# Performance work log

Hardware: AMD Instinct MI355X
Metric: run time of the kernel (lower is better)

Reference implementation:

```python
import jax, jax.numpy as jnp
import numpy as np

N_NODES = 50000
N_EDGES = 800000
DIM_IN, DIM_H, DIM_OUT = 128, 128, 64


def _init_linear(key, fan_in, fan_out):
    # kaiming-uniform-ish init, matches torch Linear scale
    lim = 1.0 / np.sqrt(fan_in)
    return jax.random.uniform(key, (fan_in, fan_out), jnp.float32, -lim, lim)


def setup_inputs() -> dict:
    key = jax.random.key(0)
    ks = jax.random.split(key, 12)
    x = jax.random.normal(ks[0], (N_NODES, DIM_IN), jnp.float32)
    edge_index = jax.random.randint(ks[1], (2, N_EDGES), 0, N_NODES, jnp.int32)
    dims = [(DIM_IN, DIM_H), (DIM_H, DIM_H), (DIM_H, DIM_OUT)]
    inp = {"x": x, "edge_index": edge_index}
    for i, (fi, fo) in enumerate(dims):
        inp[f"Wl{i}"] = _init_linear(ks[2 + 3 * i], fi, fo)   # neighbor transform
        inp[f"Wr{i}"] = _init_linear(ks[3 + 3 * i], fi, fo)   # root transform
        inp[f"b{i}"] = jnp.zeros((fo,), jnp.float32)
    return inp


def _sage_layer(x, src, dst, Wl, Wr, b):
    # mean aggregation of neighbor messages x[src] at destination nodes
    msg = x[src]                                              # [E, d]
    agg = jax.ops.segment_sum(msg, dst, num_segments=N_NODES)  # [N, d]
    cnt = jax.ops.segment_sum(jnp.ones((src.shape[0],), x.dtype), dst,
                              num_segments=N_NODES)
    mean = agg / jnp.maximum(cnt, 1.0)[:, None]               # isolated nodes -> 0
    return mean @ Wl + b + x @ Wr                              # SAGEConv


def reference(x, edge_index, Wl0, Wr0, b0, Wl1, Wr1, b1, Wl2, Wr2, b2):
    src, dst = edge_index[0], edge_index[1]
    layers = [(Wl0, Wr0, b0), (Wl1, Wr1, b1), (Wl2, Wr2, b2)]
    h = x
    for i, (Wl, Wr, b) in enumerate(layers):
        h = _sage_layer(h, src, dst, Wl, Wr, b)
        if i != len(layers) - 1:
            h = jax.nn.relu(h)  # dropout p=0.2 is identity in eval mode
    return jax.nn.log_softmax(h, axis=1), h
```

## Files before the change

kernel.cpp:

```cpp
#include <hip/hip_runtime.h>

#define N_NODES 50000
#define N_EDGES 800000
#define SCAN_BLOCKS 196
#define WIN 6250

typedef __attribute__((ext_vector_type(8))) short short8;
typedef __attribute__((ext_vector_type(4))) float f32x4;
typedef unsigned short ushort_t;
typedef unsigned int uint_t;

__device__ inline ushort_t f2bf(float f) {
    union { float f; uint_t u; } v; v.f = f;
    uint_t u = v.u;
    u += 0x7fffu + ((u >> 16) & 1u);
    return (ushort_t)(u >> 16);
}
__device__ inline float bflo(uint_t v) { return __uint_as_float(v << 16); }
__device__ inline float bfhi(uint_t v) { return __uint_as_float(v & 0xffff0000u); }
__device__ inline float bf2f(ushort_t v) { return __uint_as_float((uint_t)v << 16); }

__global__ void count_edges_mp(const int* __restrict__ ei, int* __restrict__ cnt) {
    int g = blockIdx.x & 7;
    int nb = gridDim.x >> 3;
    int bi = blockIdx.x >> 3;
    int lo = g * WIN;
    for (int e = bi * 256 + threadIdx.x; e < N_EDGES; e += nb * 256) {
        int d = ei[N_EDGES + e];
        if ((unsigned)(d - lo) < WIN) atomicAdd(&cnt[d], 1);
    }
}

__global__ void fill_csr_mp(const int* __restrict__ ei, int* __restrict__ cursor,
                            int* __restrict__ csr_src) {
    int g = blockIdx.x & 7;
    int nb = gridDim.x >> 3;
    int bi = blockIdx.x >> 3;
    int lo = g * WIN;
    for (int e = bi * 256 + threadIdx.x; e < N_EDGES; e += nb * 256) {
        int d = ei[N_EDGES + e];
        if ((unsigned)(d - lo) < WIN) {
            int p = atomicAdd(&cursor[d], 1);
            csr_src[p] = ei[e];
        }
    }
}

__global__ void block_sums(const int* __restrict__ cnt, int* __restrict__ bsum) {
    int i = blockIdx.x * 256 + threadIdx.x;
    int v = (i < N_NODES) ? cnt[i] : 0;
    for (int off = 32; off; off >>= 1) v += __shfl_down(v, off, 64);
    __shared__ int s[4];
    if ((threadIdx.x & 63) == 0) s[threadIdx.x >> 6] = v;
    __syncthreads();
    if (threadIdx.x == 0) bsum[blockIdx.x] = s[0] + s[1] + s[2] + s[3];
}

__global__ void scan_bsums(const int* __restrict__ bsum, int* __restrict__ bprefix,
                           int* __restrict__ rowstart) {
    __shared__ int s[256];
    int t = threadIdx.x;
    int v = (t < SCAN_BLOCKS) ? bsum[t] : 0;
    s[t] = v;
    __syncthreads();
    for (int off = 1; off < 256; off <<= 1) {
        int add = (t >= off) ? s[t - off] : 0;
        __syncthreads();
        s[t] += add;
        __syncthreads();
    }
    bprefix[t] = s[t] - v;
    if (t == 0) rowstart[N_NODES] = N_EDGES;
}

__global__ void apply_scan(const int* __restrict__ cnt, const int* __restrict__ bprefix,
                           int* __restrict__ rowstart, int* __restrict__ cursor) {
    __shared__ int s[256];
    int t = threadIdx.x;
    int i = blockIdx.x * 256 + t;
    int v = (i < N_NODES) ? cnt[i] : 0;
    s[t] = v;
    __syncthreads();
    for (int off = 1; off < 256; off <<= 1) {
        int add = (t >= off) ? s[t - off] : 0;
        __syncthreads();
        s[t] += add;
        __syncthreads();
    }
    int excl = s[t] - v + bprefix[blockIdx.x];
    if (i < N_NODES) { rowstart[i] = excl; cursor[i] = excl; }
}

__global__ void cvt_bf16(const float* __restrict__ in, ushort_t* __restrict__ out, int n4) {
    int i = blockIdx.x * 256 + threadIdx.x;
    if (i < n4) {
        float4 v = ((const float4*)in)[i];
        ushort4 o;
        o.x = f2bf(v.x); o.y = f2bf(v.y); o.z = f2bf(v.z); o.w = f2bf(v.w);
        ((ushort4*)out)[i] = o;
    }
}

__global__ void pack_w256(const float* __restrict__ Wl, const float* __restrict__ Wr,
                          ushort_t* __restrict__ out) {
    int idx = blockIdx.x * 256 + threadIdx.x;
    if (idx >= 8 * 8 * 64 * 8) return;
    int j = idx & 7, l = (idx >> 3) & 63, t = (idx >> 9) & 7, ks = idx >> 12;
    int n = t * 16 + (l & 15);
    int k = ks * 32 + (l >> 4) * 8 + j;
    float w = (k < 128) ? Wl[k * 128 + n] : Wr[(k - 128) * 128 + n];
    out[idx] = f2bf(w);
}

__global__ void pack_wzr(const float* __restrict__ Wl, const float* __restrict__ Wr,
                         ushort_t* __restrict__ out) {
    int idx = blockIdx.x * 256 + threadIdx.x;
    if (idx >= 4 * 8 * 64 * 8) return;
    int j = idx & 7, l = (idx >> 3) & 63, t = (idx >> 9) & 7, ks = idx >> 12;
    int n = t * 16 + (l & 15);
    int k = ks * 32 + (l >> 4) * 8 + j;
    float w = (n < 64) ? Wl[k * 64 + n] : Wr[k * 64 + (n - 64)];
    out[idx] = f2bf(w);
}

__global__ void aggregate_bf(const ushort_t* __restrict__ hbf,
                             const int* __restrict__ rowstart,
                             const int* __restrict__ csr_src,
                             ushort_t* __restrict__ meanbf) {
    int node = blockIdx.x * 4 + (threadIdx.x >> 6);
    int lane = threadIdx.x & 63;
    if (node >= N_NODES) return;
    int s0 = rowstart[node], s1 = rowstart[node + 1];
    float ax = 0.f, ay = 0.f;
    const uint_t* base = (const uint_t*)hbf;
    for (int b = s0; b < s1; b += 64) {
        int m = min(64, s1 - b);
        int idx = (lane < m) ? csr_src[b + lane] : 0;
        int j = 0;
        for (; j + 8 <= m; j += 8) {
            uint_t v0 = base[(size_t)__shfl(idx, j + 0, 64) * 64 + lane];
            uint_t v1 = base[(size_t)__shfl(idx, j + 1, 64) * 64 + lane];
            uint_t v2 = base[(size_t)__shfl(idx, j + 2, 64) * 64 + lane];
            uint_t v3 = base[(size_t)__shfl(idx, j + 3, 64) * 64 + lane];
            uint_t v4 = base[(size_t)__shfl(idx, j + 4, 64) * 64 + lane];
            uint_t v5 = base[(size_t)__shfl(idx, j + 5, 64) * 64 + lane];
            uint_t v6 = base[(size_t)__shfl(idx, j + 6, 64) * 64 + lane];
            uint_t v7 = base[(size_t)__shfl(idx, j + 7, 64) * 64 + lane];
            ax += ((bflo(v0) + bflo(v1)) + (bflo(v2) + bflo(v3)))
                + ((bflo(v4) + bflo(v5)) + (bflo(v6) + bflo(v7)));
            ay += ((bfhi(v0) + bfhi(v1)) + (bfhi(v2) + bfhi(v3)))
                + ((bfhi(v4) + bfhi(v5)) + (bfhi(v6) + bfhi(v7)));
        }
        for (; j < m; ++j) {
            uint_t v = base[(size_t)__shfl(idx, j, 64) * 64 + lane];
            ax += bflo(v);
            ay += bfhi(v);
        }
    }
    float inv = 1.0f / fmaxf((float)(s1 - s0), 1.0f);
    ax *= inv; ay *= inv;
    uint_t packed = (uint_t)f2bf(ax) | ((uint_t)f2bf(ay) << 16);
    ((uint_t*)meanbf)[(size_t)node * 64 + lane] = packed;
}

__global__ __launch_bounds__(256) void sage_gemm_pk(
    const ushort_t* __restrict__ mean_bf, const ushort_t* __restrict__ root_bf,
    const ushort_t* __restrict__ Bpk, const float* __restrict__ bias,
    ushort_t* __restrict__ out_bf) {
    int lane = threadIdx.x & 63;
    int wave = threadIdx.x >> 6;
    int row16 = lane & 15;
    int quad = lane >> 4;
    int rowBase = blockIdx.x * 64 + wave * 16;
    int arow = min(rowBase + row16, N_NODES - 1);
    const ushort_t* mrow = mean_bf + (size_t)arow * 128;
    const ushort_t* rrow = root_bf + (size_t)arow * 128;
    const short8* bp = (const short8*)Bpk + lane;

    f32x4 acc[8];
    #pragma unroll
    for (int t = 0; t < 8; ++t) { f32x4 z = {0.f, 0.f, 0.f, 0.f}; acc[t] = z; }

    #pragma unroll
    for (int ks = 0; ks < 8; ++ks) {
        const ushort_t* src = (ks < 4) ? (mrow + ks * 32 + quad * 8)
                                       : (rrow + (ks - 4) * 32 + quad * 8);
        short8 afrag = *(const short8*)src;
        #pragma unroll
        for (int t = 0; t < 8; ++t) {
            short8 bfrag = bp[(ks * 8 + t) * 64];
            acc[t] = __builtin_amdgcn_mfma_f32_16x16x32_bf16(afrag, bfrag, acc[t], 0, 0, 0);
        }
    }

    #pragma unroll
    for (int t = 0; t < 8; ++t) {
        int col = t * 16 + row16;
        float bv = bias[col];
        #pragma unroll
        for (int r = 0; r < 4; ++r) {
            int row = rowBase + quad * 4 + r;
            if (row < N_NODES) {
                float v = fmaxf(acc[t][r] + bv, 0.f);
                out_bf[(size_t)row * 128 + col] = f2bf(v);
            }
        }
    }
}

__global__ __launch_bounds__(256) void gemm_zr_pk(
    const ushort_t* __restrict__ h_bf, const ushort_t* __restrict__ Bpk,
    const float* __restrict__ bias,
    ushort_t* __restrict__ z_bf, float* __restrict__ r_f32) {
    int lane = threadIdx.x & 63;
    int wave = threadIdx.x >> 6;
    int row16 = lane & 15;
    int quad = lane >> 4;
    int rowBase = blockIdx.x * 64 + wave * 16;
    int arow = min(rowBase + row16, N_NODES - 1);
    const ushort_t* hrow = h_bf + (size_t)arow * 128;
    const short8* bp = (const short8*)Bpk + lane;

    f32x4 acc[8];
    #pragma unroll
    for (int t = 0; t < 8; ++t) { f32x4 z = {0.f, 0.f, 0.f, 0.f}; acc[t] = z; }

    #pragma unroll
    for (int ks = 0; ks < 4; ++ks) {
        short8 afrag = *(const short8*)(hrow + ks * 32 + quad * 8);
        #pragma unroll
        for (int t = 0; t < 8; ++t) {
            short8 bfrag = bp[(ks * 8 + t) * 64];
            acc[t] = __builtin_amdgcn_mfma_f32_16x16x32_bf16(afrag, bfrag, acc[t], 0, 0, 0);
        }
    }

    #pragma unroll
    for (int t = 0; t < 8; ++t) {
        int col = t * 16 + row16;
        #pragma unroll
        for (int r = 0; r < 4; ++r) {
            int row = rowBase + quad * 4 + r;
            if (row < N_NODES) {
                if (col < 64) {
                    z_bf[(size_t)row * 64 + col] = f2bf(acc[t][r]);
                } else {
                    r_f32[(size_t)row * 64 + (col - 64)] = acc[t][r] + bias[col - 64];
                }
            }
        }
    }
}

__global__ void final_agg_softmax(const ushort_t* __restrict__ z_bf,
                                  const float* __restrict__ r_f32,
                                  const int* __restrict__ rowstart,
                                  const int* __restrict__ csr_src,
                                  float* __restrict__ out) {
    int node = blockIdx.x * 4 + (threadIdx.x >> 6);
    int lane = threadIdx.x & 63;
    if (node >= N_NODES) return;
    int s0 = rowstart[node], s1 = rowstart[node + 1];
    float a = 0.f;
    for (int b = s0; b < s1; b += 64) {
        int m = min(64, s1 - b);
        int idx = (lane < m) ? csr_src[b + lane] : 0;
        int j = 0;
        for (; j + 8 <= m; j += 8) {
            float v0 = bf2f(z_bf[(size_t)__shfl(idx, j + 0, 64) * 64 + lane]);
            float v1 = bf2f(z_bf[(size_t)__shfl(idx, j + 1, 64) * 64 + lane]);
            float v2 = bf2f(z_bf[(size_t)__shfl(idx, j + 2, 64) * 64 + lane]);
            float v3 = bf2f(z_bf[(size_t)__shfl(idx, j + 3, 64) * 64 + lane]);
            float v4 = bf2f(z_bf[(size_t)__shfl(idx, j + 4, 64) * 64 + lane]);
            float v5 = bf2f(z_bf[(size_t)__shfl(idx, j + 5, 64) * 64 + lane]);
            float v6 = bf2f(z_bf[(size_t)__shfl(idx, j + 6, 64) * 64 + lane]);
            float v7 = bf2f(z_bf[(size_t)__shfl(idx, j + 7, 64) * 64 + lane]);
            a += ((v0 + v1) + (v2 + v3)) + ((v4 + v5) + (v6 + v7));
        }
        for (; j < m; ++j)
            a += bf2f(z_bf[(size_t)__shfl(idx, j, 64) * 64 + lane]);
    }
    float inv = 1.0f / fmaxf((float)(s1 - s0), 1.0f);
    float h = a * inv + r_f32[(size_t)node * 64 + lane];
    float mx = h;
    for (int off = 32; off; off >>= 1) mx = fmaxf(mx, __shfl_xor(mx, off, 64));
    float e = expf(h - mx);
    float s = e;
    for (int off = 32; off; off >>= 1) s += __shfl_xor(s, off, 64);
    float lse = mx + logf(s);
    out[(size_t)node * 64 + lane] = h - lse;
    out[(size_t)N_NODES * 64 + (size_t)node * 64 + lane] = h;
}

extern "C" void kernel_launch(void* const* d_in, const int* in_sizes, int n_in,
                              void* d_out, int out_size, void* d_ws, size_t ws_size,
                              hipStream_t stream) {
    const float* x  = (const float*)d_in[0];
    const int* ei   = (const int*)d_in[1];
    const float* Wl0 = (const float*)d_in[2];
    const float* Wr0 = (const float*)d_in[3];
    const float* b0  = (const float*)d_in[4];
    const float* Wl1 = (const float*)d_in[5];
    const float* Wr1 = (const float*)d_in[6];
    const float* b1  = (const float*)d_in[7];
    const float* Wl2 = (const float*)d_in[8];
    const float* Wr2 = (const float*)d_in[9];
    const float* b2  = (const float*)d_in[10];
    float* out = (float*)d_out;

    char* ws = (char*)d_ws;
    int* cnt      = (int*)(ws + 0x000000);
    int* rowstart = (int*)(ws + 0x040000);
    int* cursor   = (int*)(ws + 0x080000);
    int* bsum     = (int*)(ws + 0x0C0000);
    int* bprefix  = (int*)(ws + 0x0C1000);
    int* csr_src  = (int*)(ws + 0x100000);
    ushort_t* pk0 = (ushort_t*)(ws + 0x420000);
    ushort_t* pk1 = (ushort_t*)(ws + 0x440000);
    ushort_t* pkz = (ushort_t*)(ws + 0x460000);
    ushort_t* x_bf    = (ushort_t*)(ws + 0x0500000);
    ushort_t* mean_bf = (ushort_t*)(ws + 0x1200000);
    ushort_t* h_bf    = (ushort_t*)(ws + 0x1F00000);
    ushort_t* z_bf    = (ushort_t*)(ws + 0x1200000);
    float*    r_f32   = (float*)  (ws + 0x0500000);

    pack_w256<<<128, 256, 0, stream>>>(Wl0, Wr0, pk0);
    pack_w256<<<128, 256, 0, stream>>>(Wl1, Wr1, pk1);
    pack_wzr<<<64, 256, 0, stream>>>(Wl2, Wr2, pkz);

    hipMemsetAsync(cnt, 0, N_NODES * sizeof(int), stream);
    count_edges_mp<<<1024, 256, 0, stream>>>(ei, cnt);
    block_sums<<<SCAN_BLOCKS, 256, 0, stream>>>(cnt, bsum);
    scan_bsums<<<1, 256, 0, stream>>>(bsum, bprefix, rowstart);
    apply_scan<<<SCAN_BLOCKS, 256, 0, stream>>>(cnt, bprefix, rowstart, cursor);
    fill_csr_mp<<<1024, 256, 0, stream>>>(ei, cursor, csr_src);

    cvt_bf16<<<6250, 256, 0, stream>>>(x, x_bf, (N_NODES * 128) / 4);

    aggregate_bf<<<12500, 256, 0, stream>>>(x_bf, rowstart, csr_src, mean_bf);
    sage_gemm_pk<<<782, 256, 0, stream>>>(mean_bf, x_bf, pk0, b0, h_bf);

    aggregate_bf<<<12500, 256, 0, stream>>>(h_bf, rowstart, csr_src, mean_bf);
    sage_gemm_pk<<<782, 256, 0, stream>>>(mean_bf, h_bf, pk1, b1, h_bf);

    gemm_zr_pk<<<782, 256, 0, stream>>>(h_bf, pkz, b2, z_bf, r_f32);
    final_agg_softmax<<<12500, 256, 0, stream>>>(z_bf, r_f32, rowstart, csr_src, out);
}
```

Before: 329.8 us.

## Fuse mean aggregation into SAGE GEMM via LDS and vectorize gathers

Neighbor aggregation is now done inside the GEMM kernel. Each wave gathers 16 nodes' neighbor rows with 16-byte loads across four 16-lane groups and writes the bf16 means to LDS, which feed the MFMA A-fragments directly. This removes the mean_bf round trip through global memory and one launch per layer, and the buffers are reassigned so layer 1 no longer writes its output in place over its input. The final aggregation plus softmax packs 8 nodes per wave with uint4 gathers and float4 stores. The cost is only 782 blocks for the gather phase, which lowers latency hiding, and lane-divergent degree loops.

```diff
diff --git a/kernel.cpp b/kernel.cpp
--- a/kernel.cpp
+++ b/kernel.cpp
@@ -19,6 +19,11 @@
 __device__ inline float bflo(uint_t v) { return __uint_as_float(v << 16); }
 __device__ inline float bfhi(uint_t v) { return __uint_as_float(v & 0xffff0000u); }
 __device__ inline float bf2f(ushort_t v) { return __uint_as_float((uint_t)v << 16); }
+
+#define ACC8(V) { a[0] += bflo((V).x); a[1] += bfhi((V).x); \
+                  a[2] += bflo((V).y); a[3] += bfhi((V).y); \
+                  a[4] += bflo((V).z); a[5] += bfhi((V).z); \
+                  a[6] += bflo((V).w); a[7] += bfhi((V).w); }
 
 __global__ void count_edges_mp(const int* __restrict__ ei, int* __restrict__ cnt) {
     int g = blockIdx.x & 7;
@@ -123,58 +128,69 @@
     out[idx] = f2bf(w);
 }
 
-__global__ void aggregate_bf(const ushort_t* __restrict__ hbf,
-                             const int* __restrict__ rowstart,
-                             const int* __restrict__ csr_src,
-                             ushort_t* __restrict__ meanbf) {
-    int node = blockIdx.x * 4 + (threadIdx.x >> 6);
-    int lane = threadIdx.x & 63;
-    if (node >= N_NODES) return;
-    int s0 = rowstart[node], s1 = rowstart[node + 1];
-    float ax = 0.f, ay = 0.f;
-    const uint_t* base = (const uint_t*)hbf;
-    for (int b = s0; b < s1; b += 64) {
-        int m = min(64, s1 - b);
-        int idx = (lane < m) ? csr_src[b + lane] : 0;
-        int j = 0;
-        for (; j + 8 <= m; j += 8) {
-            uint_t v0 = base[(size_t)__shfl(idx, j + 0, 64) * 64 + lane];
-            uint_t v1 = base[(size_t)__shfl(idx, j + 1, 64) * 64 + lane];
-            uint_t v2 = base[(size_t)__shfl(idx, j + 2, 64) * 64 + lane];
-            uint_t v3 = base[(size_t)__shfl(idx, j + 3, 64) * 64 + lane];
-            uint_t v4 = base[(size_t)__shfl(idx, j + 4, 64) * 64 + lane];
-            uint_t v5 = base[(size_t)__shfl(idx, j + 5, 64) * 64 + lane];
-            uint_t v6 = base[(size_t)__shfl(idx, j + 6, 64) * 64 + lane];
-            uint_t v7 = base[(size_t)__shfl(idx, j + 7, 64) * 64 + lane];
-            ax += ((bflo(v0) + bflo(v1)) + (bflo(v2) + bflo(v3)))
-                + ((bflo(v4) + bflo(v5)) + (bflo(v6) + bflo(v7)));
-            ay += ((bfhi(v0) + bfhi(v1)) + (bfhi(v2) + bfhi(v3)))
-                + ((bfhi(v4) + bfhi(v5)) + (bfhi(v6) + bfhi(v7)));
-        }
-        for (; j < m; ++j) {
-            uint_t v = base[(size_t)__shfl(idx, j, 64) * 64 + lane];
-            ax += bflo(v);
-            ay += bfhi(v);
-        }
-    }
-    float inv = 1.0f / fmaxf((float)(s1 - s0), 1.0f);
-    ax *= inv; ay *= inv;
-    uint_t packed = (uint_t)f2bf(ax) | ((uint_t)f2bf(ay) << 16);
-    ((uint_t*)meanbf)[(size_t)node * 64 + lane] = packed;
-}
-
-__global__ __launch_bounds__(256) void sage_gemm_pk(
-    const ushort_t* __restrict__ mean_bf, const ushort_t* __restrict__ root_bf,
+__global__ __launch_bounds__(256) void sage_fused(
+    const ushort_t* __restrict__ feat_bf,
+    const int* __restrict__ rowstart,
+    const int* __restrict__ csr_src,
     const ushort_t* __restrict__ Bpk, const float* __restrict__ bias,
     ushort_t* __restrict__ out_bf) {
+    __shared__ uint_t mlds[64][68];
     int lane = threadIdx.x & 63;
     int wave = threadIdx.x >> 6;
+    int rowBase = blockIdx.x * 64 + wave * 16;
+    int sub = lane >> 4;
+    int sl  = lane & 15;
+    int gb  = sub << 4;
+    const uint_t* base = (const uint_t*)feat_bf;
+
+    for (int p = 0; p < 4; ++p) {
+        int node = rowBase + p * 4 + sub;
+        int s0 = 0, s1 = 0;
+        if (node < N_NODES) { s0 = rowstart[node]; s1 = rowstart[node + 1]; }
+        float a[8];
+        #pragma unroll
+        for (int k = 0; k < 8; ++k) a[k] = 0.f;
+
+        int pos = s0;
+        while (__any(pos < s1)) {
+            int m = min(16, s1 - pos);
+            int idxr = (sl < m) ? csr_src[pos + sl] : 0;
+            int mm = max(m, 0);
+            mm = max(mm, __shfl_xor(mm, 16, 64));
+            mm = max(mm, __shfl_xor(mm, 32, 64));
+            for (int j = 0; j < mm; j += 8) {
+                int  sidx[8];
+                bool vld[8];
+                #pragma unroll
+                for (int k = 0; k < 8; ++k) {
+                    int q = __shfl(idxr, (gb + j + k) & 63, 64);
+                    vld[k]  = (j + k < m);
+                    sidx[k] = vld[k] ? q : 0;
+                }
+                uint4 V[8];
+                #pragma unroll
+                for (int k = 0; k < 8; ++k)
+                    V[k] = *(const uint4*)(base + (size_t)sidx[k] * 64 + (sl << 2));
+                #pragma unroll
+                for (int k = 0; k < 8; ++k)
+                    if (vld[k]) { ACC8(V[k]); }
+            }
+            pos += 16;
+        }
+        float inv = 1.0f / fmaxf((float)(s1 - s0), 1.0f);
+        uint4 o;
+        o.x = (uint_t)f2bf(a[0] * inv) | ((uint_t)f2bf(a[1] * inv) << 16);
+        o.y = (uint_t)f2bf(a[2] * inv) | ((uint_t)f2bf(a[3] * inv) << 16);
+        o.z = (uint_t)f2bf(a[4] * inv) | ((uint_t)f2bf(a[5] * inv) << 16);
+        o.w = (uint_t)f2bf(a[6] * inv) | ((uint_t)f2bf(a[7] * inv) << 16);
+        *((uint4*)&mlds[wave * 16 + p * 4 + sub][sl << 2]) = o;
+    }
+    __syncthreads();
+
     int row16 = lane & 15;
-    int quad = lane >> 4;
-    int rowBase = blockIdx.x * 64 + wave * 16;
-    int arow = min(rowBase + row16, N_NODES - 1);
-    const ushort_t* mrow = mean_bf + (size_t)arow * 128;
-    const ushort_t* rrow = root_bf + (size_t)arow * 128;
+    int quad  = lane >> 4;
+    int arow  = min(rowBase + row16, N_NODES - 1);
+    const ushort_t* rrow = feat_bf + (size_t)arow * 128;
     const short8* bp = (const short8*)Bpk + lane;
 
     f32x4 acc[8];
@@ -183,9 +199,11 @@
 
     #pragma unroll
     for (int ks = 0; ks < 8; ++ks) {
-        const ushort_t* src = (ks < 4) ? (mrow + ks * 32 + quad * 8)
-                                       : (rrow + (ks - 4) * 32 + quad * 8);
-        short8 afrag = *(const short8*)src;
+        short8 afrag;
+        if (ks < 4)
+            afrag = *(const short8*)&mlds[wave * 16 + row16][ks * 16 + quad * 4];
+        else
+            afrag = *(const short8*)(rrow + (ks - 4) * 32 + quad * 8);
         #pragma unroll
         for (int t = 0; t < 8; ++t) {
             short8 bfrag = bp[(ks * 8 + t) * 64];
@@ -252,44 +270,75 @@
     }
 }
 
-__global__ void final_agg_softmax(const ushort_t* __restrict__ z_bf,
-                                  const float* __restrict__ r_f32,
-                                  const int* __restrict__ rowstart,
-                                  const int* __restrict__ csr_src,
-                                  float* __restrict__ out) {
-    int node = blockIdx.x * 4 + (threadIdx.x >> 6);
+__global__ __launch_bounds__(256) void final_agg_softmax2(
+    const ushort_t* __restrict__ z_bf, const float* __restrict__ r_f32,
+    const int* __restrict__ rowstart, const int* __restrict__ csr_src,
+    float* __restrict__ out) {
     int lane = threadIdx.x & 63;
+    int wave = threadIdx.x >> 6;
+    int sub = lane >> 3;
+    int sl  = lane & 7;
+    int gb  = sub << 3;
+    int node = blockIdx.x * 32 + wave * 8 + sub;
+    int s0 = 0, s1 = 0;
+    if (node < N_NODES) { s0 = rowstart[node]; s1 = rowstart[node + 1]; }
+
+    float a[8];
+    #pragma unroll
+    for (int k = 0; k < 8; ++k) a[k] = 0.f;
+    const uint_t* zb = (const uint_t*)z_bf;
+
+    int pos = s0;
+    while (__any(pos < s1)) {
+        int m = min(8, s1 - pos);
+        int idxr = (sl < m) ? csr_src[pos + sl] : 0;
+        int  sidx[8];
+        bool vld[8];
+        #pragma unroll
+        for (int k = 0; k < 8; ++k) {
+            int q = __shfl(idxr, (gb + k) & 63, 64);
+            vld[k]  = (k < m);
+            sidx[k] = vld[k] ? q : 0;
+        }
+        uint4 V[8];
+        #pragma unroll
+        for (int k = 0; k < 8; ++k)
+            V[k] = *(const uint4*)(zb + (size_t)sidx[k] * 32 + (sl << 2));
+        #pragma unroll
+        for (int k = 0; k < 8; ++k)
+            if (vld[k]) { ACC8(V[k]); }
+        pos += 8;
+    }
     if (node >= N_NODES) return;
-    int s0 = rowstart[node], s1 = rowstart[node + 1];
-    float a = 0.f;
-    for (int b = s0; b < s1; b += 64) {
-        int m = min(64, s1 - b);
-        int idx = (lane < m) ? csr_src[b + lane] : 0;
-        int j = 0;
-        for (; j + 8 <= m; j += 8) {
-            float v0 = bf2f(z_bf[(size_t)__shfl(idx, j + 0, 64) * 64 + lane]);
-            float v1 = bf2f(z_bf[(size_t)__shfl(idx, j + 1, 64) * 64 + lane]);
-            float v2 = bf2f(z_bf[(size_t)__shfl(idx, j + 2, 64) * 64 + lane]);
-            float v3 = bf2f(z_bf[(size_t)__shfl(idx, j + 3, 64) * 64 + lane]);
-            float v4 = bf2f(z_bf[(size_t)__shfl(idx, j + 4, 64) * 64 + lane]);
-            float v5 = bf2f(z_bf[(size_t)__shfl(idx, j + 5, 64) * 64 + lane]);
-            float v6 = bf2f(z_bf[(size_t)__shfl(idx, j + 6, 64) * 64 + lane]);
-            float v7 = bf2f(z_bf[(size_t)__shfl(idx, j + 7, 64) * 64 + lane]);
-            a += ((v0 + v1) + (v2 + v3)) + ((v4 + v5) + (v6 + v7));
-        }
-        for (; j < m; ++j)
-            a += bf2f(z_bf[(size_t)__shfl(idx, j, 64) * 64 + lane]);
-    }
+
     float inv = 1.0f / fmaxf((float)(s1 - s0), 1.0f);
-    float h = a * inv + r_f32[(size_t)node * 64 + lane];
-    float mx = h;
-    for (int off = 32; off; off >>= 1) mx = fmaxf(mx, __shfl_xor(mx, off, 64));
-    float e = expf(h - mx);
-    float s = e;
-    for (int off = 32; off; off >>= 1) s += __shfl_xor(s, off, 64);
+    const float4* rr = (const float4*)(r_f32 + (size_t)node * 64 + sl * 8);
+    float4 rA = rr[0], rB = rr[1];
+    float h[8];
+    h[0] = a[0] * inv + rA.x; h[1] = a[1] * inv + rA.y;
+    h[2] = a[2] * inv + rA.z; h[3] = a[3] * inv + rA.w;
+    h[4] = a[4] * inv + rB.x; h[5] = a[5] * inv + rB.y;
+    h[6] = a[6] * inv + rB.z; h[7] = a[7] * inv + rB.w;
+
+    float mx = fmaxf(fmaxf(fmaxf(h[0], h[1]), fmaxf(h[2], h[3])),
+                     fmaxf(fmaxf(h[4], h[5]), fmaxf(h[6], h[7])));
+    mx = fmaxf(mx, __shfl_xor(mx, 1, 64));
+    mx = fmaxf(mx, __shfl_xor(mx, 2, 64));
+    mx = fmaxf(mx, __shfl_xor(mx, 4, 64));
+    float s = 0.f;
+    #pragma unroll
+    for (int k = 0; k < 8; ++k) s += expf(h[k] - mx);
+    s += __shfl_xor(s, 1, 64);
+    s += __shfl_xor(s, 2, 64);
+    s += __shfl_xor(s, 4, 64);
     float lse = mx + logf(s);
-    out[(size_t)node * 64 + lane] = h - lse;
-    out[(size_t)N_NODES * 64 + (size_t)node * 64 + lane] = h;
+
+    size_t o1 = (size_t)node * 64 + sl * 8;
+    size_t o2 = (size_t)N_NODES * 64 + o1;
+    *(float4*)(out + o1)     = make_float4(h[0] - lse, h[1] - lse, h[2] - lse, h[3] - lse);
+    *(float4*)(out + o1 + 4) = make_float4(h[4] - lse, h[5] - lse, h[6] - lse, h[7] - lse);
+    *(float4*)(out + o2)     = make_float4(h[0], h[1], h[2], h[3]);
+    *(float4*)(out + o2 + 4) = make_float4(h[4], h[5], h[6], h[7]);
 }
 
 extern "C" void kernel_launch(void* const* d_in, const int* in_sizes, int n_in,
@@ -318,11 +367,11 @@
     ushort_t* pk0 = (ushort_t*)(ws + 0x420000);
     ushort_t* pk1 = (ushort_t*)(ws + 0x440000);
     ushort_t* pkz = (ushort_t*)(ws + 0x460000);
-    ushort_t* x_bf    = (ushort_t*)(ws + 0x0500000);
-    ushort_t* mean_bf = (ushort_t*)(ws + 0x1200000);
-    ushort_t* h_bf    = (ushort_t*)(ws + 0x1F00000);
-    ushort_t* z_bf    = (ushort_t*)(ws + 0x1200000);
-    float*    r_f32   = (float*)  (ws + 0x0500000);
+    ushort_t* x_bf  = (ushort_t*)(ws + 0x0500000);
+    ushort_t* h_bf  = (ushort_t*)(ws + 0x1200000);
+    ushort_t* h2_bf = (ushort_t*)(ws + 0x1F00000);
+    ushort_t* z_bf  = (ushort_t*)(ws + 0x0500000);
+    float*    r_f32 = (float*)  (ws + 0x1200000);
 
     pack_w256<<<128, 256, 0, stream>>>(Wl0, Wr0, pk0);
     pack_w256<<<128, 256, 0, stream>>>(Wl1, Wr1, pk1);
@@ -337,12 +386,10 @@
 
     cvt_bf16<<<6250, 256, 0, stream>>>(x, x_bf, (N_NODES * 128) / 4);
 
-    aggregate_bf<<<12500, 256, 0, stream>>>(x_bf, rowstart, csr_src, mean_bf);
-    sage_gemm_pk<<<782, 256, 0, stream>>>(mean_bf, x_bf, pk0, b0, h_bf);
-
-    aggregate_bf<<<12500, 256, 0, stream>>>(h_bf, rowstart, csr_src, mean_bf);
-    sage_gemm_pk<<<782, 256, 0, stream>>>(mean_bf, h_bf, pk1, b1, h_bf);
-
-    gemm_zr_pk<<<782, 256, 0, stream>>>(h_bf, pkz, b2, z_bf, r_f32);
-    final_agg_softmax<<<12500, 256, 0, stream>>>(z_bf, r_f32, rowstart, csr_src, out);
-}
+    sage_fused<<<782, 256, 0, stream>>>(x_bf, rowstart, csr_src, pk0, b0, h_bf);
+
+    sage_fused<<<782, 256, 0, stream>>>(h_bf, rowstart, csr_src, pk1, b1, h2_bf);
+
+    gemm_zr_pk<<<782, 256, 0, stream>>>(h2_bf, pkz, b2, z_bf, r_f32);
+    final_agg_softmax2<<<1563, 256, 0, stream>>>(z_bf, r_f32, rowstart, csr_src, out);
+}
```

After: 297.8 us. 1.11x faster.
